# Kernel optimization log

Measured on AMD Instinct MI355X. Metric: run time of the kernel, lower is better.

## Reference

```python
import jax, jax.numpy as jnp
import numpy as np

B, S, E, H = 4, 2048, 1024, 16
D = E // H
EPS = 1e-5


def _ln(x, g, b):
    mu = jnp.mean(x, axis=-1, keepdims=True)
    var = jnp.mean(jnp.square(x - mu), axis=-1, keepdims=True)
    return (x - mu) * jax.lax.rsqrt(var + EPS) * g + b


def setup_inputs() -> dict:
    key = jax.random.key(0)
    ks = jax.random.split(key, 12)
    s = 0.02
    return {
        "inp": jax.random.normal(ks[0], (B, S, E), jnp.float32),
        "ln1_g": jnp.ones((E,), jnp.float32),
        "ln1_b": jnp.zeros((E,), jnp.float32),
        "Wq": jax.random.normal(ks[1], (E, E), jnp.float32) * s,
        "bq": jnp.zeros((E,), jnp.float32),
        "Wk": jax.random.normal(ks[2], (E, E), jnp.float32) * s,
        "bk": jnp.zeros((E,), jnp.float32),
        "Wv": jax.random.normal(ks[3], (E, E), jnp.float32) * s,
        "bv": jnp.zeros((E,), jnp.float32),
        "Wo": jax.random.normal(ks[4], (E, E), jnp.float32) * s,
        "bo": jnp.zeros((E,), jnp.float32),
        "ln2_g": jnp.ones((E,), jnp.float32),
        "ln2_b": jnp.zeros((E,), jnp.float32),
        "W1": jax.random.normal(ks[5], (E, 2 * E), jnp.float32) * s,
        "b1": jnp.zeros((2 * E,), jnp.float32),
        "W2": jax.random.normal(ks[6], (2 * E, E), jnp.float32) * s,
        "b2": jnp.zeros((E,), jnp.float32),
    }


def reference(inp, ln1_g, ln1_b, Wq, bq, Wk, bk, Wv, bv, Wo, bo,
              ln2_g, ln2_b, W1, b1, W2, b2):
    x = _ln(inp, ln1_g, ln1_b)                      # [B,S,E]
    def heads(t):
        return t.reshape(B, S, H, D).transpose(0, 2, 1, 3)  # [B,H,S,D]
    q = heads(x @ Wq + bq)
    k = heads(x @ Wk + bk)
    v = heads(x @ Wv + bv)
    scores = jnp.einsum('bhqd,bhkd->bhqk', q, k) / jnp.sqrt(jnp.float32(D))
    attn = jax.nn.softmax(scores, axis=-1)
    out = jnp.einsum('bhqk,bhkd->bhqd', attn, v)    # [B,H,S,D]
    out = out.transpose(0, 2, 1, 3).reshape(B, S, E)
    out = out @ Wo + bo                             # dropout p=1e-4 -> identity (eval)
    x = x + out                                     # NOTE: residual from normed input (as in source)
    x = _ln(x, ln2_g, ln2_b)
    mlp = jax.nn.gelu(x @ W1 + b1, approximate=False) @ W2 + b2
    return mlp + x
```

## Files before the change

### kernel.cpp

```cpp
#include <hip/hip_runtime.h>
#include <hip/hip_bf16.h>

typedef float f32x4 __attribute__((ext_vector_type(4)));
typedef __bf16 bfv8 __attribute__((ext_vector_type(8)));

constexpr int Bc = 4, Sc = 2048, Ec = 1024, Hc = 16, Dc = 64;
constexpr int Mc = Bc * Sc;

__device__ __forceinline__ uint pkbf(float lo, float hi) {
  uint r;
  asm("v_cvt_pk_bf16_f32 %0, %1, %2" : "=v"(r) : "v"(lo), "v"(hi));
  return r;
}
__device__ __forceinline__ ushort f2bf(float f) {
  __hip_bfloat16 h = __float2bfloat16(f);
  return __builtin_bit_cast(ushort, h);
}
__device__ __forceinline__ float bf2f(ushort u) {
  return __builtin_bit_cast(float, (uint)u << 16);
}

typedef __attribute__((address_space(1))) unsigned int as1_u32;
typedef __attribute__((address_space(3))) unsigned int as3_u32;
__device__ __forceinline__ void cp16(const ushort* g, ushort* l) {
  __builtin_amdgcn_global_load_lds((as1_u32*)g, (as3_u32*)l, 16, 0, 0);
}

__global__ __launch_bounds__(256) void wcvt_all_kernel(
    const float* __restrict__ Wq, const float* __restrict__ Wk,
    const float* __restrict__ Wv, const float* __restrict__ Wo,
    const float* __restrict__ W1, const float* __restrict__ W2,
    ushort* __restrict__ WqkvT, ushort* __restrict__ WoT,
    ushort* __restrict__ W1T, ushort* __restrict__ W2T) {
  int bid = blockIdx.x;
  const float* W;
  ushort* WT;
  int K, N;
  if (bid < 1024) {
    W = Wq; WT = WqkvT; K = 1024; N = 1024;
  } else if (bid < 2048) {
    W = Wk; WT = WqkvT + (size_t)1024 * 1024; K = 1024; N = 1024; bid -= 1024;
  } else if (bid < 3072) {
    W = Wv; WT = WqkvT + (size_t)2 * 1024 * 1024; K = 1024; N = 1024; bid -= 2048;
  } else if (bid < 4096) {
    W = Wo; WT = WoT; K = 1024; N = 1024; bid -= 3072;
  } else if (bid < 6144) {
    W = W1; WT = W1T; K = 1024; N = 2048; bid -= 4096;
  } else {
    W = W2; WT = W2T; K = 2048; N = 1024; bid -= 6144;
  }
  const int nbx = K / 32;
  const int k0 = (bid % nbx) * 32, n0 = (bid / nbx) * 32;
  __shared__ float t[32][33];
  int tx = threadIdx.x, ty = threadIdx.y;
#pragma unroll
  for (int i = 0; i < 32; i += 8)
    t[ty + i][tx] = W[(size_t)(k0 + ty + i) * N + n0 + tx];
  __syncthreads();
#pragma unroll
  for (int i = 0; i < 32; i += 8)
    WT[(size_t)(n0 + ty + i) * K + k0 + tx] = f2bf(t[tx][ty + i]);
}

template <int INF32>
__global__ __launch_bounds__(256) void ln_kernel(const void* in,
                                                 const float* __restrict__ g,
                                                 const float* __restrict__ bb,
                                                 ushort* ob) {
  int row = blockIdx.x;
  int t = threadIdx.x;
  float4 x;
  if constexpr (INF32) {
    x = reinterpret_cast<const float4*>((const float*)in + (size_t)row * Ec)[t];
  } else {
    uint2 u = reinterpret_cast<const uint2*>((const ushort*)in + (size_t)row * Ec)[t];
    x.x = __builtin_bit_cast(float, u.x << 16);
    x.y = __builtin_bit_cast(float, u.x & 0xFFFF0000u);
    x.z = __builtin_bit_cast(float, u.y << 16);
    x.w = __builtin_bit_cast(float, u.y & 0xFFFF0000u);
  }
  float s = x.x + x.y + x.z + x.w;
  float q = x.x * x.x + x.y * x.y + x.z * x.z + x.w * x.w;
#pragma unroll
  for (int o = 32; o > 0; o >>= 1) {
    s += __shfl_down(s, o);
    q += __shfl_down(q, o);
  }
  __shared__ float red[10];
  int wv = t >> 6;
  if ((t & 63) == 0) { red[wv] = s; red[4 + wv] = q; }
  __syncthreads();
  if (t == 0) {
    float S = red[0] + red[1] + red[2] + red[3];
    float Q = red[4] + red[5] + red[6] + red[7];
    float mu = S * (1.f / Ec);
    float var = Q * (1.f / Ec) - mu * mu;
    red[8] = mu;
    red[9] = rsqrtf(var + 1e-5f);
  }
  __syncthreads();
  float mu = red[8], rs = red[9];
  float4 gg = reinterpret_cast<const float4*>(g)[t];
  float4 b4 = reinterpret_cast<const float4*>(bb)[t];
  float4 y;
  y.x = (x.x - mu) * rs * gg.x + b4.x;
  y.y = (x.y - mu) * rs * gg.y + b4.y;
  y.z = (x.z - mu) * rs * gg.z + b4.z;
  y.w = (x.w - mu) * rs * gg.w + b4.w;
  uint2 u;
  u.x = pkbf(y.x, y.y);
  u.y = pkbf(y.z, y.w);
  reinterpret_cast<uint2*>(ob + (size_t)row * Ec)[t] = u;
}

template <int MODE>
__global__ __launch_bounds__(256, 2) void gemm_kernel(
    int M, int N, int K, const ushort* __restrict__ A,
    const ushort* __restrict__ BT, const float* __restrict__ b0,
    const float* __restrict__ b1, const float* __restrict__ b2,
    const ushort* __restrict__ rb, float* outF, ushort* o0, ushort* o1,
    ushort* o2, float qscale) {
  __shared__ __align__(16) ushort As[2][128 * 64];
  __shared__ __align__(16) ushort Bs[2][128 * 64];
  const int tid = threadIdx.x;
  const int lane = tid & 63, wave = tid >> 6;
  const int wr = wave >> 1, wc = wave & 1;
  const int fr = lane & 15, fq = lane >> 4;
  const int nx = gridDim.x;
  int flat = blockIdx.x + nx * blockIdx.y;
  int cpx = (nx * gridDim.y) >> 3;
  int work = (flat & 7) * cpx + (flat >> 3);
  const int n0 = (work % nx) * 128, m0 = (work / nx) * 128;

  f32x4 acc[4][4];
#pragma unroll
  for (int i = 0; i < 4; i++)
#pragma unroll
    for (int j = 0; j < 4; j++) acc[i][j] = f32x4{0.f, 0.f, 0.f, 0.f};

  const int srow = tid >> 3;
  const int sslot = tid & 7;

  auto STAGE = [&](int p, int k0) {
#pragma unroll
    for (int c = 0; c < 4; ++c) {
      int row = c * 32 + srow;
      int scol = (sslot ^ (row & 7)) * 8;
      cp16(A + (size_t)(m0 + row) * K + k0 + scol,
           &As[p][(c * 256 + wave * 64) * 8]);
      cp16(BT + (size_t)(n0 + row) * K + k0 + scol,
           &Bs[p][(c * 256 + wave * 64) * 8]);
    }
  };

  STAGE(0, 0);
  const int nt = K >> 6;
  for (int kt = 0; kt < nt; ++kt) {
    const int p = kt & 1;
    if (kt + 1 < nt) {
      STAGE(p ^ 1, (kt + 1) << 6);
      asm volatile("s_waitcnt vmcnt(8)" ::: "memory");
    } else {
      asm volatile("s_waitcnt vmcnt(0)" ::: "memory");
    }
    __builtin_amdgcn_s_barrier();
#pragma unroll
    for (int kk = 0; kk < 2; ++kk) {
      bfv8 af[4], bf[4];
#pragma unroll
      for (int m = 0; m < 4; m++) {
        int row = wr * 64 + m * 16 + fr;
        af[m] = *reinterpret_cast<const bfv8*>(
            &As[p][row * 64 + (((kk * 4 + fq) ^ (fr & 7)) * 8)]);
      }
#pragma unroll
      for (int n = 0; n < 4; n++) {
        int row = wc * 64 + n * 16 + fr;
        bf[n] = *reinterpret_cast<const bfv8*>(
            &Bs[p][row * 64 + (((kk * 4 + fq) ^ (fr & 7)) * 8)]);
      }
      __builtin_amdgcn_s_setprio(1);
#pragma unroll
      for (int m = 0; m < 4; m++)
#pragma unroll
        for (int n = 0; n < 4; n++)
          acc[m][n] =
              __builtin_amdgcn_mfma_f32_16x16x32_bf16(af[m], bf[n], acc[m][n], 0, 0, 0);
      __builtin_amdgcn_s_setprio(0);
    }
    __builtin_amdgcn_sched_barrier(0);
    __builtin_amdgcn_s_barrier();
  }

#pragma unroll
  for (int m = 0; m < 4; m++) {
#pragma unroll
    for (int n = 0; n < 4; n++) {
      const int row0 = m0 + wr * 64 + m * 16 + fq * 4;
      const int col = n0 + wc * 64 + n * 16 + fr;
      if constexpr (MODE == 0) {
        const int region = col >> 10, c1 = col & (Ec - 1);
        const int b = row0 >> 11, s0 = row0 & (Sc - 1);
        const int h = c1 >> 6, d = c1 & (Dc - 1);
        const float bb = (region == 0 ? b0 : region == 1 ? b1 : b2)[c1];
        if (region == 2) {
          uint2 u;
          u.x = pkbf(acc[m][n][0] + bb, acc[m][n][1] + bb);
          u.y = pkbf(acc[m][n][2] + bb, acc[m][n][3] + bb);
          *reinterpret_cast<uint2*>(
              &o2[(((size_t)b * Hc + h) * Dc + d) * Sc + s0]) = u;
        } else {
          ushort* dst = region ? o1 : o0;
          const float sc = region ? 1.f : qscale;
#pragma unroll
          for (int r = 0; r < 4; r++)
            dst[(((size_t)b * Hc + h) * Sc + s0 + r) * Dc + d] =
                f2bf((acc[m][n][r] + bb) * sc);
        }
      } else {
        const float bb = b0[col];
#pragma unroll
        for (int r = 0; r < 4; r++) {
          int row = row0 + r;
          size_t idx = (size_t)row * N + col;
          float vacc = acc[m][n][r] + bb + bf2f(rb[idx]);
          if constexpr (MODE == 1) {
            o0[idx] = f2bf(vacc);
          } else {
            outF[idx] = vacc;
          }
        }
      }
    }
  }
}

template <int MODE>
__global__ __launch_bounds__(512, 2) void gemm256_kernel(
    int M, int N, int K, const ushort* __restrict__ A,
    const ushort* __restrict__ BT, const float* __restrict__ b0,
    ushort* o0, float qscale) {
  __shared__ __align__(16) ushort As[2][256 * 64];
  __shared__ __align__(16) ushort Bs[2][256 * 64];
  const int tid = threadIdx.x;
  const int lane = tid & 63, wave = tid >> 6;
  const int wr = wave >> 2, wc = wave & 3;
  const int fr = lane & 15, fq = lane >> 4;
  const int nx = gridDim.x;
  int flat = blockIdx.x + nx * blockIdx.y;
  int cpx = (nx * gridDim.y) >> 3;
  int work = (flat & 7) * cpx + (flat >> 3);
  const int n0 = (work % nx) * 256, m0 = (work / nx) * 256;

  f32x4 acc[8][4];
#pragma unroll
  for (int i = 0; i < 8; i++)
#pragma unroll
    for (int j = 0; j < 4; j++) acc[i][j] = f32x4{0.f, 0.f, 0.f, 0.f};

  const int srow = tid >> 3;
  const int sslot = tid & 7;

  auto STAGE = [&](int p, int k0) {
#pragma unroll
    for (int c = 0; c < 4; ++c) {
      int row = c * 64 + srow;
      int scol = (sslot ^ (row & 7)) * 8;
      cp16(A + (size_t)(m0 + row) * K + k0 + scol,
           &As[p][(c * 64 + wave * 8) * 64]);
      cp16(BT + (size_t)(n0 + row) * K + k0 + scol,
           &Bs[p][(c * 64 + wave * 8) * 64]);
    }
  };

  STAGE(0, 0);
  const int nt = K >> 6;
  for (int kt = 0; kt < nt; ++kt) {
    const int p = kt & 1;
    if (kt + 1 < nt) {
      STAGE(p ^ 1, (kt + 1) << 6);
      asm volatile("s_waitcnt vmcnt(8)" ::: "memory");
    } else {
      asm volatile("s_waitcnt vmcnt(0)" ::: "memory");
    }
    __builtin_amdgcn_s_barrier();
#pragma unroll
    for (int kk = 0; kk < 2; ++kk) {
      bfv8 bfr[4];
#pragma unroll
      for (int n = 0; n < 4; ++n) {
        int row = wc * 64 + n * 16 + fr;
        bfr[n] = *reinterpret_cast<const bfv8*>(
            &Bs[p][row * 64 + (((kk * 4 + fq) ^ (row & 7)) * 8)]);
      }
#pragma unroll
      for (int mh = 0; mh < 2; ++mh) {
        bfv8 af[4];
#pragma unroll
        for (int mm = 0; mm < 4; ++mm) {
          int row = wr * 128 + (mh * 4 + mm) * 16 + fr;
          af[mm] = *reinterpret_cast<const bfv8*>(
              &As[p][row * 64 + (((kk * 4 + fq) ^ (row & 7)) * 8)]);
        }
        __builtin_amdgcn_s_setprio(1);
#pragma unroll
        for (int mm = 0; mm < 4; ++mm)
#pragma unroll
          for (int n = 0; n < 4; ++n)
            acc[mh * 4 + mm][n] = __builtin_amdgcn_mfma_f32_16x16x32_bf16(
                af[mm], bfr[n], acc[mh * 4 + mm][n], 0, 0, 0);
        __builtin_amdgcn_s_setprio(0);
        if (!(kk == 1 && mh == 1)) __builtin_amdgcn_s_barrier();
      }
    }
    __builtin_amdgcn_sched_barrier(0);
    __builtin_amdgcn_s_barrier();
  }

#pragma unroll
  for (int m = 0; m < 8; m++) {
#pragma unroll
    for (int n = 0; n < 4; n++) {
      const int row0 = m0 + wr * 128 + m * 16 + fq * 4;
      const int col = n0 + wc * 64 + n * 16 + fr;
      const float bb = b0[col];
#pragma unroll
      for (int r = 0; r < 4; r++) {
        float vacc = acc[m][n][r] + bb;
        vacc = 0.5f * vacc * (1.f + erff(vacc * 0.70710678118f));
        o0[(size_t)(row0 + r) * N + col] = f2bf(vacc);
      }
    }
  }
}

__global__ __launch_bounds__(256) void attn_kernel(const ushort* __restrict__ q,
                                                   const ushort* __restrict__ k,
                                                   const ushort* __restrict__ vt,
                                                   ushort* __restrict__ o) {
  int flat = blockIdx.x;
  int swz = (flat & 7) * 128 + (flat >> 3);
  const int qb = swz & 15;
  const int bh = swz >> 4;
  const int tid = threadIdx.x, lane = tid & 63, wave = tid >> 6;
  const int fr = lane & 15, fq = lane >> 4;
  const size_t base = (size_t)bh * Sc * Dc;
  const int q0 = qb * 128 + wave * 32;

  __shared__ __align__(16) ushort Ks[2][64 * 64];
  __shared__ __align__(16) ushort Vt[2][64 * 64];
  __shared__ __align__(16) ushort Ps[4][16 * 64];

  bfv8 qf0[2], qf1[2];
#pragma unroll
  for (int f = 0; f < 2; ++f) {
    const ushort* qp = q + base + (size_t)(q0 + f * 16 + fr) * Dc + fq * 8;
    qf0[f] = *reinterpret_cast<const bfv8*>(qp);
    qf1[f] = *reinterpret_cast<const bfv8*>(qp + 32);
  }

  const bfv8 ones = __builtin_bit_cast(bfv8, uint4{0x3F803F80u, 0x3F803F80u,
                                                  0x3F803F80u, 0x3F803F80u});

  f32x4 oacc[2][4];
  f32x4 oaccL[2];
#pragma unroll
  for (int f = 0; f < 2; ++f) {
    oaccL[f] = f32x4{0.f, 0.f, 0.f, 0.f};
#pragma unroll
    for (int d = 0; d < 4; ++d) oacc[f][d] = f32x4{0.f, 0.f, 0.f, 0.f};
  }
  float mrow[2] = {-3e38f, -3e38f};

  const int r8 = tid >> 3;
  const int c8 = tid & 7;

  auto STAGE = [&](int p, int key0) {
#pragma unroll
    for (int i = 0; i < 2; ++i) {
      int row = i * 32 + r8;
      int sc = (c8 ^ (row & 7)) * 8;
      cp16(k + base + (size_t)(key0 + row) * Dc + sc,
           &Ks[p][i * 2048 + wave * 512]);
      cp16(vt + base + (size_t)row * Sc + key0 + sc,
           &Vt[p][i * 2048 + wave * 512]);
    }
  };

  const int sA = (fq ^ (fr & 7)) * 8;
  const int sB = ((fq + 4) ^ (fr & 7)) * 8;

  const int pswz = 2 * (fr & 7);
  const int pr0 = fr * 64 + ((fq * 2) ^ pswz) * 4;
  const int pr1 = fr * 64 + ((fq * 2 + 8) ^ pswz) * 4;

  STAGE(0, 0);
  constexpr int NT = Sc / 64;
  for (int kt = 0; kt < NT; ++kt) {
    const int p = kt & 1;
    if (kt + 1 < NT) {
      STAGE(p ^ 1, (kt + 1) * 64);
      asm volatile("s_waitcnt vmcnt(4)" ::: "memory");
    } else {
      asm volatile("s_waitcnt vmcnt(0)" ::: "memory");
    }
    __builtin_amdgcn_s_barrier();

    bfv8 kf0[4], kf1[4], vf0[4], vf1[4];
#pragma unroll
    for (int t = 0; t < 4; ++t) {
      int e = (t * 16 + fr) * 64;
      kf0[t] = *reinterpret_cast<const bfv8*>(&Ks[p][e + sA]);
      kf1[t] = *reinterpret_cast<const bfv8*>(&Ks[p][e + sB]);
      vf0[t] = *reinterpret_cast<const bfv8*>(&Vt[p][e + sA]);
      vf1[t] = *reinterpret_cast<const bfv8*>(&Vt[p][e + sB]);
    }

#pragma unroll
    for (int f = 0; f < 2; ++f) {
      f32x4 sf[4];
      __builtin_amdgcn_s_setprio(1);
#pragma unroll
      for (int t = 0; t < 4; ++t) {
        sf[t] = f32x4{0.f, 0.f, 0.f, 0.f};
        sf[t] = __builtin_amdgcn_mfma_f32_16x16x32_bf16(kf0[t], qf0[f], sf[t], 0, 0, 0);
        sf[t] = __builtin_amdgcn_mfma_f32_16x16x32_bf16(kf1[t], qf1[f], sf[t], 0, 0, 0);
      }
      __builtin_amdgcn_s_setprio(0);
      float mt0 = fmaxf(fmaxf(sf[0][0], sf[0][1]), fmaxf(sf[0][2], sf[0][3]));
      float mt1 = fmaxf(fmaxf(sf[1][0], sf[1][1]), fmaxf(sf[1][2], sf[1][3]));
      float mt2 = fmaxf(fmaxf(sf[2][0], sf[2][1]), fmaxf(sf[2][2], sf[2][3]));
      float mt3 = fmaxf(fmaxf(sf[3][0], sf[3][1]), fmaxf(sf[3][2], sf[3][3]));
      float pmax = fmaxf(fmaxf(mt0, mt1), fmaxf(mt2, mt3));
      float m = mrow[f];
      float mnew = m;
      if (!__all(pmax <= m + 8.f)) {
        float mt = fmaxf(pmax, __shfl_xor(pmax, 16));
        mt = fmaxf(mt, __shfl_xor(mt, 32));
        mnew = fmaxf(m, mt);
        float alpha = __builtin_amdgcn_exp2f(m - mnew);
        float ar[4];
#pragma unroll
        for (int r = 0; r < 4; ++r) ar[r] = __shfl(alpha, fq * 4 + r);
#pragma unroll
        for (int d = 0; d < 4; ++d)
#pragma unroll
          for (int r = 0; r < 4; ++r) oacc[f][d][r] *= ar[r];
#pragma unroll
        for (int r = 0; r < 4; ++r) oaccL[f][r] *= ar[r];
        mrow[f] = mnew;
      }
      ushort* pw = &Ps[wave][0];
#pragma unroll
      for (int t = 0; t < 4; ++t) {
        uint2 pu;
        pu.x = pkbf(__builtin_amdgcn_exp2f(sf[t][0] - mnew),
                    __builtin_amdgcn_exp2f(sf[t][1] - mnew));
        pu.y = pkbf(__builtin_amdgcn_exp2f(sf[t][2] - mnew),
                    __builtin_amdgcn_exp2f(sf[t][3] - mnew));
        int us = fr * 64 + ((t * 4 + fq) ^ pswz) * 4;
        *reinterpret_cast<uint2*>(&pw[us]) = pu;
      }
      bfv8 pf0 = *reinterpret_cast<const bfv8*>(&pw[pr0]);
      bfv8 pf1 = *reinterpret_cast<const bfv8*>(&pw[pr1]);
      __builtin_amdgcn_s_setprio(1);
#pragma unroll
      for (int d = 0; d < 4; ++d) {
        oacc[f][d] = __builtin_amdgcn_mfma_f32_16x16x32_bf16(pf0, vf0[d], oacc[f][d], 0, 0, 0);
        oacc[f][d] = __builtin_amdgcn_mfma_f32_16x16x32_bf16(pf1, vf1[d], oacc[f][d], 0, 0, 0);
      }
      oaccL[f] = __builtin_amdgcn_mfma_f32_16x16x32_bf16(pf0, ones, oaccL[f], 0, 0, 0);
      oaccL[f] = __builtin_amdgcn_mfma_f32_16x16x32_bf16(pf1, ones, oaccL[f], 0, 0, 0);
      __builtin_amdgcn_s_setprio(0);
    }
    __builtin_amdgcn_sched_barrier(0);
    __builtin_amdgcn_s_barrier();
  }

  const int b = bh >> 4, h = bh & 15;
#pragma unroll
  for (int f = 0; f < 2; ++f) {
    float linv[4];
#pragma unroll
    for (int r = 0; r < 4; ++r) linv[r] = 1.f / oaccL[f][r];
#pragma unroll
    for (int d = 0; d < 4; ++d)
#pragma unroll
      for (int r = 0; r < 4; ++r) {
        int sIdx = q0 + f * 16 + fq * 4 + r;
        o[((size_t)(b * Sc + sIdx)) * Ec + h * 64 + d * 16 + fr] =
            f2bf(oacc[f][d][r] * linv[r]);
      }
  }
}

extern "C" void kernel_launch(void* const* d_in, const int* in_sizes, int n_in,
                              void* d_out, int out_size, void* d_ws, size_t ws_size,
                              hipStream_t stream) {
  const float* inp = (const float*)d_in[0];
  const float* ln1g = (const float*)d_in[1];
  const float* ln1b = (const float*)d_in[2];
  const float* Wq = (const float*)d_in[3];
  const float* bq = (const float*)d_in[4];
  const float* Wk = (const float*)d_in[5];
  const float* bk = (const float*)d_in[6];
  const float* Wv = (const float*)d_in[7];
  const float* bv = (const float*)d_in[8];
  const float* Wo = (const float*)d_in[9];
  const float* bo = (const float*)d_in[10];
  const float* ln2g = (const float*)d_in[11];
  const float* ln2b = (const float*)d_in[12];
  const float* W1 = (const float*)d_in[13];
  const float* b1 = (const float*)d_in[14];
  const float* W2 = (const float*)d_in[15];
  const float* b2 = (const float*)d_in[16];

  char* wsb = (char*)d_ws;
  size_t off = 0;
  auto alloc = [&](size_t bytes) {
    char* p = wsb + off;
    off += (bytes + 255) & ~(size_t)255;
    return p;
  };
  ushort* xb = (ushort*)alloc((size_t)Mc * Ec * 2);
  ushort* x2b = (ushort*)alloc((size_t)Mc * Ec * 2);
  ushort* x3b = (ushort*)alloc((size_t)Mc * Ec * 2);
  ushort* qbuf = (ushort*)alloc((size_t)Mc * Ec * 2);
  ushort* kbuf = (ushort*)alloc((size_t)Mc * Ec * 2);
  ushort* vtbuf = (ushort*)alloc((size_t)Mc * Ec * 2);
  ushort* abuf = (ushort*)alloc((size_t)Mc * Ec * 2);
  ushort* h1 = (ushort*)alloc((size_t)Mc * 2 * Ec * 2);
  ushort* WqkvT = (ushort*)alloc((size_t)3 * Ec * Ec * 2);
  ushort* WoT = (ushort*)alloc((size_t)Ec * Ec * 2);
  ushort* W1T = (ushort*)alloc((size_t)Ec * 2 * Ec * 2);
  ushort* W2T = (ushort*)alloc((size_t)Ec * 2 * Ec * 2);
  (void)in_sizes; (void)n_in; (void)out_size; (void)ws_size;

  wcvt_all_kernel<<<8192, dim3(32, 8), 0, stream>>>(Wq, Wk, Wv, Wo, W1, W2,
                                                    WqkvT, WoT, W1T, W2T);

  ln_kernel<1><<<Mc, 256, 0, stream>>>(inp, ln1g, ln1b, xb);

  gemm_kernel<0><<<dim3(3 * Ec / 128, Mc / 128), 256, 0, stream>>>(
      Mc, 3 * Ec, Ec, xb, WqkvT, bq, bk, bv, nullptr, nullptr, qbuf, kbuf,
      vtbuf, 0.18033688f);

  attn_kernel<<<Bc * Hc * (Sc / 128), 256, 0, stream>>>(qbuf, kbuf, vtbuf, abuf);

  gemm_kernel<1><<<dim3(Ec / 128, Mc / 128), 256, 0, stream>>>(
      Mc, Ec, Ec, abuf, WoT, bo, nullptr, nullptr, xb, nullptr, x2b, nullptr,
      nullptr, 1.f);

  ln_kernel<0><<<Mc, 256, 0, stream>>>(x2b, ln2g, ln2b, x3b);

  gemm256_kernel<2><<<dim3(2 * Ec / 256, Mc / 256), 512, 0, stream>>>(
      Mc, 2 * Ec, Ec, x3b, W1T, b1, h1, 1.f);

  gemm_kernel<3><<<dim3(Ec / 128, Mc / 128), 256, 0, stream>>>(
      Mc, Ec, 2 * Ec, h1, W2T, b2, nullptr, nullptr, x3b, (float*)d_out,
      nullptr, nullptr, nullptr, 1.f);
}
```

Before: 333.5 us.

## Split attention work across eight waves with sixteen query rows each

The attention block grows from 256 to 512 threads, so each wave handles 16 query rows instead of 32. The K/V tile staging is spread over twice as many threads, each issuing one copy per tensor, and the wait count is adjusted to match. This cuts per-wave register pressure and adds parallelism to hide latency. The cost is that each wave now loads its K/V fragments from LDS for only half as much MFMA work, which doubles LDS fragment reads per tile, and the block uses more P scratch space in LDS.

```diff
diff --git a/kernel.cpp b/kernel.cpp
--- a/kernel.cpp
+++ b/kernel.cpp
@@ -334,7 +334,7 @@
   }
 }
 
-__global__ __launch_bounds__(256) void attn_kernel(const ushort* __restrict__ q,
+__global__ __launch_bounds__(512) void attn_kernel(const ushort* __restrict__ q,
                                                    const ushort* __restrict__ k,
                                                    const ushort* __restrict__ vt,
                                                    ushort* __restrict__ o) {
@@ -345,46 +345,36 @@
   const int tid = threadIdx.x, lane = tid & 63, wave = tid >> 6;
   const int fr = lane & 15, fq = lane >> 4;
   const size_t base = (size_t)bh * Sc * Dc;
-  const int q0 = qb * 128 + wave * 32;
+  const int q0 = qb * 128 + wave * 16;
 
   __shared__ __align__(16) ushort Ks[2][64 * 64];
   __shared__ __align__(16) ushort Vt[2][64 * 64];
-  __shared__ __align__(16) ushort Ps[4][16 * 64];
-
-  bfv8 qf0[2], qf1[2];
-#pragma unroll
-  for (int f = 0; f < 2; ++f) {
-    const ushort* qp = q + base + (size_t)(q0 + f * 16 + fr) * Dc + fq * 8;
-    qf0[f] = *reinterpret_cast<const bfv8*>(qp);
-    qf1[f] = *reinterpret_cast<const bfv8*>(qp + 32);
+  __shared__ __align__(16) ushort Ps[8][16 * 64];
+
+  bfv8 qf0, qf1;
+  {
+    const ushort* qp = q + base + (size_t)(q0 + fr) * Dc + fq * 8;
+    qf0 = *reinterpret_cast<const bfv8*>(qp);
+    qf1 = *reinterpret_cast<const bfv8*>(qp + 32);
   }
 
   const bfv8 ones = __builtin_bit_cast(bfv8, uint4{0x3F803F80u, 0x3F803F80u,
                                                   0x3F803F80u, 0x3F803F80u});
 
-  f32x4 oacc[2][4];
-  f32x4 oaccL[2];
-#pragma unroll
-  for (int f = 0; f < 2; ++f) {
-    oaccL[f] = f32x4{0.f, 0.f, 0.f, 0.f};
-#pragma unroll
-    for (int d = 0; d < 4; ++d) oacc[f][d] = f32x4{0.f, 0.f, 0.f, 0.f};
-  }
-  float mrow[2] = {-3e38f, -3e38f};
+  f32x4 oacc[4];
+  f32x4 oaccL;
+  oaccL = f32x4{0.f, 0.f, 0.f, 0.f};
+#pragma unroll
+  for (int d = 0; d < 4; ++d) oacc[d] = f32x4{0.f, 0.f, 0.f, 0.f};
+  float mrow = -3e38f;
 
   const int r8 = tid >> 3;
   const int c8 = tid & 7;
 
   auto STAGE = [&](int p, int key0) {
-#pragma unroll
-    for (int i = 0; i < 2; ++i) {
-      int row = i * 32 + r8;
-      int sc = (c8 ^ (row & 7)) * 8;
-      cp16(k + base + (size_t)(key0 + row) * Dc + sc,
-           &Ks[p][i * 2048 + wave * 512]);
-      cp16(vt + base + (size_t)row * Sc + key0 + sc,
-           &Vt[p][i * 2048 + wave * 512]);
-    }
+    int sc = (c8 ^ (r8 & 7)) * 8;
+    cp16(k + base + (size_t)(key0 + r8) * Dc + sc, &Ks[p][wave * 512]);
+    cp16(vt + base + (size_t)r8 * Sc + key0 + sc, &Vt[p][wave * 512]);
   };
 
   const int sA = (fq ^ (fr & 7)) * 8;
@@ -400,7 +390,7 @@
     const int p = kt & 1;
     if (kt + 1 < NT) {
       STAGE(p ^ 1, (kt + 1) * 64);
-      asm volatile("s_waitcnt vmcnt(4)" ::: "memory");
+      asm volatile("s_waitcnt vmcnt(2)" ::: "memory");
     } else {
       asm volatile("s_waitcnt vmcnt(0)" ::: "memory");
     }
@@ -416,82 +406,76 @@
       vf1[t] = *reinterpret_cast<const bfv8*>(&Vt[p][e + sB]);
     }
 
-#pragma unroll
-    for (int f = 0; f < 2; ++f) {
-      f32x4 sf[4];
-      __builtin_amdgcn_s_setprio(1);
-#pragma unroll
-      for (int t = 0; t < 4; ++t) {
-        sf[t] = f32x4{0.f, 0.f, 0.f, 0.f};
-        sf[t] = __builtin_amdgcn_mfma_f32_16x16x32_bf16(kf0[t], qf0[f], sf[t], 0, 0, 0);
-        sf[t] = __builtin_amdgcn_mfma_f32_16x16x32_bf16(kf1[t], qf1[f], sf[t], 0, 0, 0);
-      }
-      __builtin_amdgcn_s_setprio(0);
-      float mt0 = fmaxf(fmaxf(sf[0][0], sf[0][1]), fmaxf(sf[0][2], sf[0][3]));
-      float mt1 = fmaxf(fmaxf(sf[1][0], sf[1][1]), fmaxf(sf[1][2], sf[1][3]));
-      float mt2 = fmaxf(fmaxf(sf[2][0], sf[2][1]), fmaxf(sf[2][2], sf[2][3]));
-      float mt3 = fmaxf(fmaxf(sf[3][0], sf[3][1]), fmaxf(sf[3][2], sf[3][3]));
-      float pmax = fmaxf(fmaxf(mt0, mt1), fmaxf(mt2, mt3));
-      float m = mrow[f];
-      float mnew = m;
-      if (!__all(pmax <= m + 8.f)) {
-        float mt = fmaxf(pmax, __shfl_xor(pmax, 16));
-        mt = fmaxf(mt, __shfl_xor(mt, 32));
-        mnew = fmaxf(m, mt);
-        float alpha = __builtin_amdgcn_exp2f(m - mnew);
-        float ar[4];
-#pragma unroll
-        for (int r = 0; r < 4; ++r) ar[r] = __shfl(alpha, fq * 4 + r);
-#pragma unroll
-        for (int d = 0; d < 4; ++d)
-#pragma unroll
-          for (int r = 0; r < 4; ++r) oacc[f][d][r] *= ar[r];
-#pragma unroll
-        for (int r = 0; r < 4; ++r) oaccL[f][r] *= ar[r];
-        mrow[f] = mnew;
-      }
-      ushort* pw = &Ps[wave][0];
-#pragma unroll
-      for (int t = 0; t < 4; ++t) {
-        uint2 pu;
-        pu.x = pkbf(__builtin_amdgcn_exp2f(sf[t][0] - mnew),
-                    __builtin_amdgcn_exp2f(sf[t][1] - mnew));
-        pu.y = pkbf(__builtin_amdgcn_exp2f(sf[t][2] - mnew),
-                    __builtin_amdgcn_exp2f(sf[t][3] - mnew));
-        int us = fr * 64 + ((t * 4 + fq) ^ pswz) * 4;
-        *reinterpret_cast<uint2*>(&pw[us]) = pu;
-      }
-      bfv8 pf0 = *reinterpret_cast<const bfv8*>(&pw[pr0]);
-      bfv8 pf1 = *reinterpret_cast<const bfv8*>(&pw[pr1]);
-      __builtin_amdgcn_s_setprio(1);
-#pragma unroll
-      for (int d = 0; d < 4; ++d) {
-        oacc[f][d] = __builtin_amdgcn_mfma_f32_16x16x32_bf16(pf0, vf0[d], oacc[f][d], 0, 0, 0);
-        oacc[f][d] = __builtin_amdgcn_mfma_f32_16x16x32_bf16(pf1, vf1[d], oacc[f][d], 0, 0, 0);
-      }
-      oaccL[f] = __builtin_amdgcn_mfma_f32_16x16x32_bf16(pf0, ones, oaccL[f], 0, 0, 0);
-      oaccL[f] = __builtin_amdgcn_mfma_f32_16x16x32_bf16(pf1, ones, oaccL[f], 0, 0, 0);
-      __builtin_amdgcn_s_setprio(0);
-    }
+    f32x4 sf[4];
+    __builtin_amdgcn_s_setprio(1);
+#pragma unroll
+    for (int t = 0; t < 4; ++t) {
+      sf[t] = f32x4{0.f, 0.f, 0.f, 0.f};
+      sf[t] = __builtin_amdgcn_mfma_f32_16x16x32_bf16(kf0[t], qf0, sf[t], 0, 0, 0);
+      sf[t] = __builtin_amdgcn_mfma_f32_16x16x32_bf16(kf1[t], qf1, sf[t], 0, 0, 0);
+    }
+    __builtin_amdgcn_s_setprio(0);
+    float mt0 = fmaxf(fmaxf(sf[0][0], sf[0][1]), fmaxf(sf[0][2], sf[0][3]));
+    float mt1 = fmaxf(fmaxf(sf[1][0], sf[1][1]), fmaxf(sf[1][2], sf[1][3]));
+    float mt2 = fmaxf(fmaxf(sf[2][0], sf[2][1]), fmaxf(sf[2][2], sf[2][3]));
+    float mt3 = fmaxf(fmaxf(sf[3][0], sf[3][1]), fmaxf(sf[3][2], sf[3][3]));
+    float pmax = fmaxf(fmaxf(mt0, mt1), fmaxf(mt2, mt3));
+    float mnew = mrow;
+    if (!__all(pmax <= mrow + 8.f)) {
+      float mt = fmaxf(pmax, __shfl_xor(pmax, 16));
+      mt = fmaxf(mt, __shfl_xor(mt, 32));
+      mnew = fmaxf(mrow, mt);
+      float alpha = __builtin_amdgcn_exp2f(mrow - mnew);
+      float ar[4];
+#pragma unroll
+      for (int r = 0; r < 4; ++r) ar[r] = __shfl(alpha, fq * 4 + r);
+#pragma unroll
+      for (int d = 0; d < 4; ++d)
+#pragma unroll
+        for (int r = 0; r < 4; ++r) oacc[d][r] *= ar[r];
+#pragma unroll
+      for (int r = 0; r < 4; ++r) oaccL[r] *= ar[r];
+      mrow = mnew;
+    }
+    ushort* pw = &Ps[wave][0];
+#pragma unroll
+    for (int t = 0; t < 4; ++t) {
+      uint2 pu;
+      pu.x = pkbf(__builtin_amdgcn_exp2f(sf[t][0] - mnew),
+                  __builtin_amdgcn_exp2f(sf[t][1] - mnew));
+      pu.y = pkbf(__builtin_amdgcn_exp2f(sf[t][2] - mnew),
+                  __builtin_amdgcn_exp2f(sf[t][3] - mnew));
+      int us = fr * 64 + ((t * 4 + fq) ^ pswz) * 4;
+      *reinterpret_cast<uint2*>(&pw[us]) = pu;
+    }
+    bfv8 pf0 = *reinterpret_cast<const bfv8*>(&pw[pr0]);
+    bfv8 pf1 = *reinterpret_cast<const bfv8*>(&pw[pr1]);
+    __builtin_amdgcn_s_setprio(1);
+#pragma unroll
+    for (int d = 0; d < 4; ++d) {
+      oacc[d] = __builtin_amdgcn_mfma_f32_16x16x32_bf16(pf0, vf0[d], oacc[d], 0, 0, 0);
+      oacc[d] = __builtin_amdgcn_mfma_f32_16x16x32_bf16(pf1, vf1[d], oacc[d], 0, 0, 0);
+    }
+    oaccL = __builtin_amdgcn_mfma_f32_16x16x32_bf16(pf0, ones, oaccL, 0, 0, 0);
+    oaccL = __builtin_amdgcn_mfma_f32_16x16x32_bf16(pf1, ones, oaccL, 0, 0, 0);
+    __builtin_amdgcn_s_setprio(0);
+
     __builtin_amdgcn_sched_barrier(0);
     __builtin_amdgcn_s_barrier();
   }
 
   const int b = bh >> 4, h = bh & 15;
-#pragma unroll
-  for (int f = 0; f < 2; ++f) {
-    float linv[4];
-#pragma unroll
-    for (int r = 0; r < 4; ++r) linv[r] = 1.f / oaccL[f][r];
-#pragma unroll
-    for (int d = 0; d < 4; ++d)
-#pragma unroll
-      for (int r = 0; r < 4; ++r) {
-        int sIdx = q0 + f * 16 + fq * 4 + r;
-        o[((size_t)(b * Sc + sIdx)) * Ec + h * 64 + d * 16 + fr] =
-            f2bf(oacc[f][d][r] * linv[r]);
-      }
-  }
+  float linv[4];
+#pragma unroll
+  for (int r = 0; r < 4; ++r) linv[r] = 1.f / oaccL[r];
+#pragma unroll
+  for (int d = 0; d < 4; ++d)
+#pragma unroll
+    for (int r = 0; r < 4; ++r) {
+      int sIdx = q0 + fq * 4 + r;
+      o[((size_t)(b * Sc + sIdx)) * Ec + h * 64 + d * 16 + fr] =
+          f2bf(oacc[d][r] * linv[r]);
+    }
 }
 
 extern "C" void kernel_launch(void* const* d_in, const int* in_sizes, int n_in,
@@ -545,7 +529,7 @@
       Mc, 3 * Ec, Ec, xb, WqkvT, bq, bk, bv, nullptr, nullptr, qbuf, kbuf,
       vtbuf, 0.18033688f);
 
-  attn_kernel<<<Bc * Hc * (Sc / 128), 256, 0, stream>>>(qbuf, kbuf, vtbuf, abuf);
+  attn_kernel<<<Bc * Hc * (Sc / 128), 512, 0, stream>>>(qbuf, kbuf, vtbuf, abuf);
 
   gemm_kernel<1><<<dim3(Ec / 128, Mc / 128), 256, 0, stream>>>(
       Mc, Ec, Ec, abuf, WoT, bo, nullptr, nullptr, xb, nullptr, x2b, nullptr,
```

New measurement: 318.9 us. 1.05x faster.
